# Kernel tuning notes

Hardware: AMD Instinct MI355X
Metric: run time of the kernel (lower is better)

Reference implementation:

```python
import jax, jax.numpy as jnp
import numpy as np


def setup_inputs() -> dict:
    key = jax.random.key(0)
    ks = jax.random.split(key, 5)
    B, N, H, S, D = 1, 256, 4, 256, 32
    q = jax.random.normal(ks[0], (B, N, H, S, D), dtype=jnp.float32)
    k = jax.random.normal(ks[1], (B, N, H, S, D), dtype=jnp.float32)
    v = jax.random.normal(ks[2], (B, N, H, S, D), dtype=jnp.float32)
    mask_bias = jax.random.normal(ks[3], (B, N, 1, 1, S), dtype=jnp.float32)
    triangle_bias = jax.random.normal(ks[4], (B, 1, H, S, S), dtype=jnp.float32)
    return {"q": q, "k": k, "v": v, "mask_bias": mask_bias, "triangle_bias": triangle_bias}


def reference(q, k, v, mask_bias, triangle_bias):
    # q,k,v: [B, N, H, S, D]; mask_bias: [B, N, 1, 1, S]; triangle_bias: [B, 1, H, S, S]
    D = q.shape[-1]
    sm_scale = 1.0 / jnp.sqrt(jnp.asarray(D, dtype=q.dtype))
    # scores: [B, N, H, S, S] (query index s attends over key index t)
    scores = jnp.einsum("bnhsd,bnhtd->bnhst", q, k) * sm_scale
    scores = scores + mask_bias + triangle_bias  # broadcast add of both biases
    p = jax.nn.softmax(scores, axis=-1)
    out = jnp.einsum("bnhst,bnhtd->bnhsd", p, v)
    return out
```

## Files before the change

kernel.cpp:

```cpp
#include <hip/hip_runtime.h>

typedef __bf16 bf16;
typedef bf16 bf16x8 __attribute__((ext_vector_type(8)));
typedef bf16 bf16x4 __attribute__((ext_vector_type(4)));
typedef float f32x4 __attribute__((ext_vector_type(4)));

#define SEQ 256
#define DH  32
#define VT_PAD 264
#define P_PAD  40

__global__ __launch_bounds__(256, 4) void attn_mfma_kernel(
    const float* __restrict__ q,
    const float* __restrict__ k,
    const float* __restrict__ v,
    const float* __restrict__ mask_bias,
    const float* __restrict__ tri_bias,
    float* __restrict__ out)
{
    __shared__ bf16 Vt[DH][VT_PAD];
    __shared__ bf16 Pb[4][64][P_PAD];

    const int tid  = threadIdx.x;
    const int wave = tid >> 6;
    const int lane = tid & 63;
    const int l15  = lane & 15;
    const int quad = lane >> 4;

    const int inst = blockIdx.x;
    const int n    = inst >> 2;
    const int h    = inst & 3;

    const float* qb = q + (size_t)inst * SEQ * DH;
    const float* kb = k + (size_t)inst * SEQ * DH;
    const float* vb = v + (size_t)inst * SEQ * DH;
    const float* mb = mask_bias + (size_t)n * SEQ;
    const float* tb = tri_bias + (size_t)h * SEQ * SEQ;

    const float K1    = 0.17677669529663687f * 1.44269504088896f;
    const float LOG2E = 1.44269504088896f;

    #pragma unroll
    for (int i = 0; i < 8; ++i) {
        int idx = i * 256 + tid;
        int t = idx >> 3;
        int d = (idx & 7) * 4;
        float4 tv = ((const float4*)vb)[idx];
        Vt[d + 0][t] = (bf16)tv.x;
        Vt[d + 1][t] = (bf16)tv.y;
        Vt[d + 2][t] = (bf16)tv.z;
        Vt[d + 3][t] = (bf16)tv.w;
    }
    __syncthreads();

    const int s_base = wave * 64;
    bf16x8 qfrag[4];
    #pragma unroll
    for (int st = 0; st < 4; ++st) {
        const float* p = qb + (size_t)(s_base + st * 16 + l15) * DH + quad * 8;
        float4 a = ((const float4*)p)[0];
        float4 b = ((const float4*)p)[1];
        bf16x8 f;
        f[0] = (bf16)a.x; f[1] = (bf16)a.y; f[2] = (bf16)a.z; f[3] = (bf16)a.w;
        f[4] = (bf16)b.x; f[5] = (bf16)b.y; f[6] = (bf16)b.z; f[7] = (bf16)b.w;
        qfrag[st] = f;
    }

    f32x4 oacc[4][2];
    #pragma unroll
    for (int st = 0; st < 4; ++st)
        #pragma unroll
        for (int dt = 0; dt < 2; ++dt)
            oacc[st][dt] = (f32x4){0.f, 0.f, 0.f, 0.f};
    float lpart[4] = {0.f, 0.f, 0.f, 0.f};

    const f32x4 zero4 = {0.f, 0.f, 0.f, 0.f};

    for (int c = 0; c < 8; ++c) {
        #pragma unroll
        for (int half = 0; half < 2; ++half) {
            const int mt = c * 2 + half;
            const int t0 = mt * 16;

            const float* kp = kb + (size_t)(t0 + l15) * DH + quad * 8;
            float4 ka = ((const float4*)kp)[0];
            float4 kc = ((const float4*)kp)[1];
            bf16x8 kfrag;
            kfrag[0] = (bf16)ka.x; kfrag[1] = (bf16)ka.y;
            kfrag[2] = (bf16)ka.z; kfrag[3] = (bf16)ka.w;
            kfrag[4] = (bf16)kc.x; kfrag[5] = (bf16)kc.y;
            kfrag[6] = (bf16)kc.z; kfrag[7] = (bf16)kc.w;

            float4 mk = *(const float4*)(mb + t0 + quad * 4);
            float4 tr[4];
            #pragma unroll
            for (int st = 0; st < 4; ++st) {
                const float* tp = tb + (size_t)(s_base + st * 16 + l15) * SEQ + t0 + quad * 4;
                tr[st] = *(const float4*)tp;
            }
            float mkl0 = mk.x * LOG2E, mkl1 = mk.y * LOG2E;
            float mkl2 = mk.z * LOG2E, mkl3 = mk.w * LOG2E;

            f32x4 cf[4];
            #pragma unroll
            for (int st = 0; st < 4; ++st)
                cf[st] = __builtin_amdgcn_mfma_f32_16x16x32_bf16(kfrag, qfrag[st], zero4, 0, 0, 0);

            #pragma unroll
            for (int st = 0; st < 4; ++st) {
                float p0 = __builtin_amdgcn_exp2f(fmaf(tr[st].x, LOG2E, fmaf(cf[st][0], K1, mkl0)));
                float p1 = __builtin_amdgcn_exp2f(fmaf(tr[st].y, LOG2E, fmaf(cf[st][1], K1, mkl1)));
                float p2 = __builtin_amdgcn_exp2f(fmaf(tr[st].z, LOG2E, fmaf(cf[st][2], K1, mkl2)));
                float p3 = __builtin_amdgcn_exp2f(fmaf(tr[st].w, LOG2E, fmaf(cf[st][3], K1, mkl3)));
                lpart[st] += (p0 + p1) + (p2 + p3);
                bf16x4 pk;
                pk[0] = (bf16)p0; pk[1] = (bf16)p1; pk[2] = (bf16)p2; pk[3] = (bf16)p3;
                *(bf16x4*)&Pb[wave][st * 16 + l15][half * 16 + quad * 4] = pk;
            }
        }

        bf16x8 vf[2];
        #pragma unroll
        for (int dt = 0; dt < 2; ++dt)
            vf[dt] = *(const bf16x8*)&Vt[dt * 16 + l15][c * 32 + quad * 8];
        #pragma unroll
        for (int st = 0; st < 4; ++st) {
            bf16x8 pf = *(const bf16x8*)&Pb[wave][st * 16 + l15][quad * 8];
            #pragma unroll
            for (int dt = 0; dt < 2; ++dt)
                oacc[st][dt] = __builtin_amdgcn_mfma_f32_16x16x32_bf16(pf, vf[dt], oacc[st][dt], 0, 0, 0);
        }
    }

    float linv[4];
    #pragma unroll
    for (int st = 0; st < 4; ++st) {
        float x = lpart[st];
        x += __shfl_xor(x, 16);
        x += __shfl_xor(x, 32);
        linv[st] = 1.0f / x;
    }

    float* ob = out + (size_t)inst * SEQ * DH;
    #pragma unroll
    for (int st = 0; st < 4; ++st) {
        #pragma unroll
        for (int r = 0; r < 4; ++r) {
            float invr = __shfl(linv[st], quad * 4 + r);
            int s = s_base + st * 16 + quad * 4 + r;
            float* orow = ob + (size_t)s * DH;
            orow[l15]      = oacc[st][0][r] * invr;
            orow[16 + l15] = oacc[st][1][r] * invr;
        }
    }
}

extern "C" void kernel_launch(void* const* d_in, const int* in_sizes, int n_in,
                              void* d_out, int out_size, void* d_ws, size_t ws_size,
                              hipStream_t stream) {
    const float* q    = (const float*)d_in[0];
    const float* k    = (const float*)d_in[1];
    const float* v    = (const float*)d_in[2];
    const float* mask = (const float*)d_in[3];
    const float* tri  = (const float*)d_in[4];
    float* out = (float*)d_out;

    attn_mfma_kernel<<<dim3(256 * 4), dim3(256), 0, stream>>>(q, k, v, mask, tri, out);
}
```

Measured before the change: 178.2 us.

## Pre-convert triangle bias to bf16, stage Q/K/V and bias tiles in LDS, 512-thread blocks

A separate pre-pass converts the triangle bias to bf16 in a padded workspace, halving the bias traffic that every (n,h) block re-reads. The main kernel now uses 512 threads with 32 query rows per wave. It stages Q, K and transposed V in shared memory and streams bias chunks through an LDS tile with register prefetch, reusing that tile for the P values. Output is staged through LDS for coalesced float4 stores. The cost is an extra launch, two barriers per chunk, larger shared memory use, and rounding the bias to bf16 before the softmax.

```diff
diff --git a/kernel.cpp b/kernel.cpp
--- a/kernel.cpp
+++ b/kernel.cpp
@@ -4,22 +4,34 @@
 typedef bf16 bf16x8 __attribute__((ext_vector_type(8)));
 typedef bf16 bf16x4 __attribute__((ext_vector_type(4)));
 typedef float f32x4 __attribute__((ext_vector_type(4)));
+typedef unsigned int u32;
+typedef u32 u32x4 __attribute__((ext_vector_type(4)));
 
 #define SEQ 256
 #define DH  32
-#define VT_PAD 264
-#define P_PAD  40
+#define TRI_PAD 288
+#define KROW 40
+#define VROW 264
 
-__global__ __launch_bounds__(256, 4) void attn_mfma_kernel(
+__global__ void tri_cvt_kernel(const float* __restrict__ tri, bf16* __restrict__ tri16) {
+    const int row = blockIdx.x;
+    const int tid = threadIdx.x;
+    tri16[(size_t)row * TRI_PAD + tid] = (bf16)tri[(size_t)row * SEQ + tid];
+}
+
+__global__ __launch_bounds__(512, 4) void attn_mfma2_kernel(
     const float* __restrict__ q,
     const float* __restrict__ k,
     const float* __restrict__ v,
     const float* __restrict__ mask_bias,
-    const float* __restrict__ tri_bias,
+    const bf16*  __restrict__ tri16,
     float* __restrict__ out)
 {
-    __shared__ bf16 Vt[DH][VT_PAD];
-    __shared__ bf16 Pb[4][64][P_PAD];
+    __shared__ __align__(16) char arena[57856];
+    bf16*  Kc = (bf16*)arena;
+    bf16*  Vt = (bf16*)(arena + 20480);
+    bf16*  Tc = (bf16*)(arena + 37376);
+    float* Ob = (float*)arena;
 
     const int tid  = threadIdx.x;
     const int wave = tid >> 6;
@@ -35,123 +47,127 @@
     const float* kb = k + (size_t)inst * SEQ * DH;
     const float* vb = v + (size_t)inst * SEQ * DH;
     const float* mb = mask_bias + (size_t)n * SEQ;
-    const float* tb = tri_bias + (size_t)h * SEQ * SEQ;
+    const bf16*  tb = tri16 + (size_t)h * SEQ * TRI_PAD;
+    float* ob = out + (size_t)inst * SEQ * DH;
 
     const float K1    = 0.17677669529663687f * 1.44269504088896f;
     const float LOG2E = 1.44269504088896f;
+    const f32x4 zero4 = {0.f, 0.f, 0.f, 0.f};
 
     #pragma unroll
-    for (int i = 0; i < 8; ++i) {
-        int idx = i * 256 + tid;
-        int t = idx >> 3;
-        int d = (idx & 7) * 4;
-        float4 tv = ((const float4*)vb)[idx];
-        Vt[d + 0][t] = (bf16)tv.x;
-        Vt[d + 1][t] = (bf16)tv.y;
-        Vt[d + 2][t] = (bf16)tv.z;
-        Vt[d + 3][t] = (bf16)tv.w;
+    for (int i = 0; i < 4; ++i) {
+        int p  = i * 512 + tid;
+        int s  = p >> 3;
+        int d4 = (p & 7) * 4;
+        float4 fq = ((const float4*)qb)[p];
+        float4 fk = ((const float4*)kb)[p];
+        float4 fv = ((const float4*)vb)[p];
+        bf16x4 q4; q4[0]=(bf16)fq.x; q4[1]=(bf16)fq.y; q4[2]=(bf16)fq.z; q4[3]=(bf16)fq.w;
+        *(bf16x4*)&Tc[s * KROW + d4] = q4;
+        bf16x4 k4; k4[0]=(bf16)fk.x; k4[1]=(bf16)fk.y; k4[2]=(bf16)fk.z; k4[3]=(bf16)fk.w;
+        *(bf16x4*)&Kc[s * KROW + d4] = k4;
+        Vt[(d4 + 0) * VROW + s] = (bf16)fv.x;
+        Vt[(d4 + 1) * VROW + s] = (bf16)fv.y;
+        Vt[(d4 + 2) * VROW + s] = (bf16)fv.z;
+        Vt[(d4 + 3) * VROW + s] = (bf16)fv.w;
     }
+
+    const int p0 = tid, p1 = tid + 512;
+    u32x4 R0 = *(const u32x4*)(tb + (size_t)(p0 >> 2) * TRI_PAD + (p0 & 3) * 8);
+    u32x4 R1 = *(const u32x4*)(tb + (size_t)(p1 >> 2) * TRI_PAD + (p1 & 3) * 8);
+
     __syncthreads();
 
-    const int s_base = wave * 64;
-    bf16x8 qfrag[4];
+    bf16x8 qfrag[2];
+    qfrag[0] = *(const bf16x8*)&Tc[(wave * 32 + l15) * KROW + quad * 8];
+    qfrag[1] = *(const bf16x8*)&Tc[(wave * 32 + 16 + l15) * KROW + quad * 8];
+
+    f32x4 oacc[2][2];
     #pragma unroll
-    for (int st = 0; st < 4; ++st) {
-        const float* p = qb + (size_t)(s_base + st * 16 + l15) * DH + quad * 8;
-        float4 a = ((const float4*)p)[0];
-        float4 b = ((const float4*)p)[1];
-        bf16x8 f;
-        f[0] = (bf16)a.x; f[1] = (bf16)a.y; f[2] = (bf16)a.z; f[3] = (bf16)a.w;
-        f[4] = (bf16)b.x; f[5] = (bf16)b.y; f[6] = (bf16)b.z; f[7] = (bf16)b.w;
-        qfrag[st] = f;
-    }
-
-    f32x4 oacc[4][2];
-    #pragma unroll
-    for (int st = 0; st < 4; ++st)
+    for (int st = 0; st < 2; ++st)
         #pragma unroll
         for (int dt = 0; dt < 2; ++dt)
-            oacc[st][dt] = (f32x4){0.f, 0.f, 0.f, 0.f};
-    float lpart[4] = {0.f, 0.f, 0.f, 0.f};
-
-    const f32x4 zero4 = {0.f, 0.f, 0.f, 0.f};
+            oacc[st][dt] = zero4;
+    float lpart[2] = {0.f, 0.f};
 
     for (int c = 0; c < 8; ++c) {
+        __syncthreads();
+        *(u32x4*)&Tc[(p0 >> 2) * KROW + (p0 & 3) * 8] = R0;
+        *(u32x4*)&Tc[(p1 >> 2) * KROW + (p1 & 3) * 8] = R1;
+        if (c < 7) {
+            R0 = *(const u32x4*)(tb + (size_t)(p0 >> 2) * TRI_PAD + (c + 1) * 32 + (p0 & 3) * 8);
+            R1 = *(const u32x4*)(tb + (size_t)(p1 >> 2) * TRI_PAD + (c + 1) * 32 + (p1 & 3) * 8);
+        }
+        __syncthreads();
+
         #pragma unroll
         for (int half = 0; half < 2; ++half) {
-            const int mt = c * 2 + half;
-            const int t0 = mt * 16;
-
-            const float* kp = kb + (size_t)(t0 + l15) * DH + quad * 8;
-            float4 ka = ((const float4*)kp)[0];
-            float4 kc = ((const float4*)kp)[1];
-            bf16x8 kfrag;
-            kfrag[0] = (bf16)ka.x; kfrag[1] = (bf16)ka.y;
-            kfrag[2] = (bf16)ka.z; kfrag[3] = (bf16)ka.w;
-            kfrag[4] = (bf16)kc.x; kfrag[5] = (bf16)kc.y;
-            kfrag[6] = (bf16)kc.z; kfrag[7] = (bf16)kc.w;
-
-            float4 mk = *(const float4*)(mb + t0 + quad * 4);
-            float4 tr[4];
-            #pragma unroll
-            for (int st = 0; st < 4; ++st) {
-                const float* tp = tb + (size_t)(s_base + st * 16 + l15) * SEQ + t0 + quad * 4;
-                tr[st] = *(const float4*)tp;
-            }
+            const int t0h = c * 32 + half * 16;
+            bf16x8 kfrag = *(const bf16x8*)&Kc[(t0h + l15) * KROW + quad * 8];
+            float4 mk = *(const float4*)(mb + t0h + quad * 4);
             float mkl0 = mk.x * LOG2E, mkl1 = mk.y * LOG2E;
             float mkl2 = mk.z * LOG2E, mkl3 = mk.w * LOG2E;
 
-            f32x4 cf[4];
             #pragma unroll
-            for (int st = 0; st < 4; ++st)
-                cf[st] = __builtin_amdgcn_mfma_f32_16x16x32_bf16(kfrag, qfrag[st], zero4, 0, 0, 0);
-
-            #pragma unroll
-            for (int st = 0; st < 4; ++st) {
-                float p0 = __builtin_amdgcn_exp2f(fmaf(tr[st].x, LOG2E, fmaf(cf[st][0], K1, mkl0)));
-                float p1 = __builtin_amdgcn_exp2f(fmaf(tr[st].y, LOG2E, fmaf(cf[st][1], K1, mkl1)));
-                float p2 = __builtin_amdgcn_exp2f(fmaf(tr[st].z, LOG2E, fmaf(cf[st][2], K1, mkl2)));
-                float p3 = __builtin_amdgcn_exp2f(fmaf(tr[st].w, LOG2E, fmaf(cf[st][3], K1, mkl3)));
-                lpart[st] += (p0 + p1) + (p2 + p3);
-                bf16x4 pk;
-                pk[0] = (bf16)p0; pk[1] = (bf16)p1; pk[2] = (bf16)p2; pk[3] = (bf16)p3;
-                *(bf16x4*)&Pb[wave][st * 16 + l15][half * 16 + quad * 4] = pk;
+            for (int st = 0; st < 2; ++st) {
+                const int srow = wave * 32 + st * 16 + l15;
+                bf16x4 t4 = *(const bf16x4*)&Tc[srow * KROW + half * 16 + quad * 4];
+                f32x4 cf = __builtin_amdgcn_mfma_f32_16x16x32_bf16(kfrag, qfrag[st], zero4, 0, 0, 0);
+                float s0 = fmaf(cf[0], K1, fmaf((float)t4[0], LOG2E, mkl0));
+                float s1 = fmaf(cf[1], K1, fmaf((float)t4[1], LOG2E, mkl1));
+                float s2 = fmaf(cf[2], K1, fmaf((float)t4[2], LOG2E, mkl2));
+                float s3 = fmaf(cf[3], K1, fmaf((float)t4[3], LOG2E, mkl3));
+                float e0 = __builtin_amdgcn_exp2f(s0);
+                float e1 = __builtin_amdgcn_exp2f(s1);
+                float e2 = __builtin_amdgcn_exp2f(s2);
+                float e3 = __builtin_amdgcn_exp2f(s3);
+                lpart[st] += (e0 + e1) + (e2 + e3);
+                bf16x4 pk; pk[0]=(bf16)e0; pk[1]=(bf16)e1; pk[2]=(bf16)e2; pk[3]=(bf16)e3;
+                *(bf16x4*)&Tc[srow * KROW + half * 16 + quad * 4] = pk;
             }
         }
 
-        bf16x8 vf[2];
+        bf16x8 vf0 = *(const bf16x8*)&Vt[(l15) * VROW + c * 32 + quad * 8];
+        bf16x8 vf1 = *(const bf16x8*)&Vt[(16 + l15) * VROW + c * 32 + quad * 8];
         #pragma unroll
-        for (int dt = 0; dt < 2; ++dt)
-            vf[dt] = *(const bf16x8*)&Vt[dt * 16 + l15][c * 32 + quad * 8];
-        #pragma unroll
-        for (int st = 0; st < 4; ++st) {
-            bf16x8 pf = *(const bf16x8*)&Pb[wave][st * 16 + l15][quad * 8];
-            #pragma unroll
-            for (int dt = 0; dt < 2; ++dt)
-                oacc[st][dt] = __builtin_amdgcn_mfma_f32_16x16x32_bf16(pf, vf[dt], oacc[st][dt], 0, 0, 0);
+        for (int st = 0; st < 2; ++st) {
+            bf16x8 pf = *(const bf16x8*)&Tc[(wave * 32 + st * 16 + l15) * KROW + quad * 8];
+            oacc[st][0] = __builtin_amdgcn_mfma_f32_16x16x32_bf16(pf, vf0, oacc[st][0], 0, 0, 0);
+            oacc[st][1] = __builtin_amdgcn_mfma_f32_16x16x32_bf16(pf, vf1, oacc[st][1], 0, 0, 0);
         }
     }
 
-    float linv[4];
+    float linv[2];
     #pragma unroll
-    for (int st = 0; st < 4; ++st) {
+    for (int st = 0; st < 2; ++st) {
         float x = lpart[st];
         x += __shfl_xor(x, 16);
         x += __shfl_xor(x, 32);
         linv[st] = 1.0f / x;
     }
 
-    float* ob = out + (size_t)inst * SEQ * DH;
+    __syncthreads();
+
     #pragma unroll
-    for (int st = 0; st < 4; ++st) {
+    for (int st = 0; st < 2; ++st) {
         #pragma unroll
         for (int r = 0; r < 4; ++r) {
             float invr = __shfl(linv[st], quad * 4 + r);
-            int s = s_base + st * 16 + quad * 4 + r;
-            float* orow = ob + (size_t)s * DH;
-            orow[l15]      = oacc[st][0][r] * invr;
-            orow[16 + l15] = oacc[st][1][r] * invr;
+            int s = wave * 32 + st * 16 + quad * 4 + r;
+            Ob[s * 36 + l15]      = oacc[st][0][r] * invr;
+            Ob[s * 36 + 16 + l15] = oacc[st][1][r] * invr;
         }
+    }
+    __syncthreads();
+
+    #pragma unroll
+    for (int i = 0; i < 4; ++i) {
+        int p  = i * 512 + tid;
+        int s  = p >> 3;
+        int d4 = (p & 7) * 4;
+        f32x4 o = *(const f32x4*)&Ob[s * 36 + d4];
+        float4 w; w.x = o[0]; w.y = o[1]; w.z = o[2]; w.w = o[3];
+        ((float4*)ob)[p] = w;
     }
 }
 
@@ -165,5 +181,8 @@
     const float* tri  = (const float*)d_in[4];
     float* out = (float*)d_out;
 
-    attn_mfma_kernel<<<dim3(256 * 4), dim3(256), 0, stream>>>(q, k, v, mask, tri, out);
+    bf16* tri16 = (bf16*)d_ws;
+
+    tri_cvt_kernel<<<dim3(4 * SEQ), dim3(SEQ), 0, stream>>>(tri, tri16);
+    attn_mfma2_kernel<<<dim3(SEQ * 4), dim3(512), 0, stream>>>(q, k, v, mask, tri16, out);
 }
```

Result: slower. 196.6 us (+10.3%).
